# Optimization experiments

Hardware: AMD Instinct MI355X
Metric: run time of the kernel (lower is better)

The kernel has to match this reference:

```python
import jax, jax.numpy as jnp
import numpy as np

PATCH = 3
ALPHA = 0.1


def _unfold3x3(x):
    # x: [B, C, H, W] -> [B, C*9, H, W], torch F.unfold with k=3, pad=1, stride=1
    B, C, H, W = x.shape
    p = PATCH // 2
    xp = jnp.pad(x, ((0, 0), (0, 0), (p, p), (p, p)))
    shifts = [xp[:, :, i:i + H, j:j + W] for i in range(PATCH) for j in range(PATCH)]
    # torch unfold orders (C, kh, kw); ordering is irrelevant for the dot-product
    # correlation, but we match it anyway: stack kernel positions after channel.
    out = jnp.stack(shifts, axis=2)  # [B, C, 9, H, W]
    return out.reshape(B, C * PATCH * PATCH, H, W)


def setup_inputs() -> dict:
    key = jax.random.key(0)
    k1, k2 = jax.random.split(key)
    x_lab = jax.random.normal(k1, (4, 3, 64, 64), dtype=jnp.float32)
    feature = jax.random.normal(k2, (4, 64, 64, 64), dtype=jnp.float32)
    return {"x_lab": x_lab, "feature": feature}


def reference(x_lab, feature):
    # scale_factor=1 and feature already at (H, W): both interpolates are identity.
    B, _, H, W = x_lab.shape
    N = H * W
    x_ab = x_lab.reshape(B, 3, N).transpose(0, 2, 1)          # [B, N, 3]
    lf = _unfold3x3(feature).reshape(B, -1, N)                 # [B, C*9, N]
    corr = jnp.einsum('bcn,bcm->bnm', lf, lf)                  # [B, N, N]
    attn = jax.nn.softmax(corr / ALPHA, axis=-1)
    weighted = jnp.einsum('bnm,bmc->bnc', attn, x_ab)          # [B, N, 3]
    return weighted.transpose(0, 2, 1).reshape(B, 3, H, W)
```

## Files before the change

### kernel.cpp

```cpp
#include <hip/hip_runtime.h>


#define NPIX 4096
#define ROWB  (528 * 16)
#define SCALE 10.0f
#define XCH   1024

typedef __attribute__((ext_vector_type(8))) short bf16x8;
typedef __attribute__((ext_vector_type(4))) float f32x4;

#define MF(a, b, c) __builtin_amdgcn_mfma_f32_16x16x32_bf16(a, b, c, 0, 0, 0)

__device__ __forceinline__ uint4 pack8(const float* v) {
    unsigned h[8];
#pragma unroll
    for (int j = 0; j < 8; ++j) {
        unsigned u = __float_as_uint(v[j]);
        u = u + 0x7fffu + ((u >> 16) & 1u);
        h[j] = u >> 16;
    }
    return (uint4){h[0] | (h[1] << 16), h[2] | (h[3] << 16),
                   h[4] | (h[5] << 16), h[6] | (h[7] << 16)};
}

__device__ __forceinline__ void load_row(const float* fr, int kc, int x, float* L) {
#pragma unroll
    for (int j = 0; j < 8; ++j) L[j] = fr[(size_t)(kc * 8 + j) * NPIX + x];
}

#define MG(T, DBASE, KT) do {                                                 \
    _Pragma("unroll")                                                         \
    for (int dx = 0; dx < 3; ++dx)                                            \
        _Pragma("unroll")                                                     \
        for (int ks = 0; ks < 2; ++ks)                                        \
            acc[T][KT] = MF(AF[((DBASE) + dx) * 2 + ks], B2[ks][dx], acc[T][KT]); \
} while (0)

#define RETIRE(S, myv) do {                                                   \
    _Pragma("unroll")                                                         \
    for (int kt = 0; kt < 4; ++kt) {                                          \
        const int kx = kt * 16 + nl;                                          \
        const float xv0 = xls[(myv) * 64 + kx];                               \
        const float xv1 = xls[XCH + (myv) * 64 + kx];                         \
        const float xv2 = xls[2 * XCH + (myv) * 64 + kx];                     \
        _Pragma("unroll")                                                     \
        for (int rg = 0; rg < 4; ++rg) {                                      \
            const float e = __expf(fmaf(acc[S][kt][rg], SCALE, negM[rg]));    \
            l_[rg] += e;                                                      \
            A0[rg] = fmaf(e, xv0, A0[rg]);                                    \
            A1[rg] = fmaf(e, xv1, A1[rg]);                                    \
            A2[rg] = fmaf(e, xv2, A2[rg]);                                    \
        }                                                                     \
        acc[S][kt] = (f32x4){0.f, 0.f, 0.f, 0.f};                             \
    }                                                                         \
} while (0)

#define STEP(RM, SN, SR, tt) do {                                             \
    const int t_ = (tt);                                                      \
    if (t_ <= 15) {                                                           \
        const int g2 = R0 + 1 + t_;                                           \
        if (g2 < 64) {                                                        \
            float L[8];                                                       \
            load_row(featb + g2 * 64, kc0, x, L);                             \
            *(uint4*)(ring + (SR) * ROWB + wu0) = pack8(L);                   \
            load_row(featb + g2 * 64, kc1, x, L);                             \
            *(uint4*)(ring + (SR) * ROWB + wu1) = pack8(L);                   \
        } else {                                                              \
            *(uint4*)(ring + (SR) * ROWB + wu0) = (uint4){0u, 0u, 0u, 0u};    \
            *(uint4*)(ring + (SR) * ROWB + wu1) = (uint4){0u, 0u, 0u, 0u};    \
        }                                                                     \
    }                                                                         \
    {                                                                         \
        const char* base = ring + (RM) * ROWB + bu;                           \
        _Pragma("unroll")                                                     \
        for (int kt = 0; kt < 4; ++kt) {                                      \
            bf16x8 B2[2][3];                                                  \
            _Pragma("unroll")                                                 \
            for (int ks = 0; ks < 2; ++ks) {                                  \
                const char* p = base + (ks * 264 + kt * 16) * 16;             \
                B2[ks][0] = *(const bf16x8*)(p);                              \
                B2[ks][1] = *(const bf16x8*)(p + 16);                         \
                B2[ks][2] = *(const bf16x8*)(p + 32);                         \
            }                                                                 \
            if (t_ >= 2)              MG(SR, 6, kt);        \
            if (t_ >= 1 && t_ <= 16)  MG(RM, 3, kt);        \
            if (t_ <= 15)             MG(SN, 0, kt);        \
        }                                                                     \
    }                                                                         \
    if (t_ >= 2) RETIRE(SR, t_ - 2);                                          \
    if (t_ < 17) __syncthreads();                                             \
} while (0)

__global__ __launch_bounds__(256)
__attribute__((amdgpu_waves_per_eu(2)))
void nlwa_fused(const float* __restrict__ x_lab,
                const float* __restrict__ feature,
                float4* __restrict__ ws)
{
    __shared__ __align__(16) char ring[3 * ROWB];
    __shared__ float xls[3 * XCH];
    __shared__ float part[3][4][64];
    __shared__ float ssq[3][64];

    const int tid = threadIdx.x;
    const int b = blockIdx.x >> 8;
    const int rem = blockIdx.x & 255;
    const int ny = rem >> 2, kq = rem & 3;
    const int R0 = kq * 16;
    const int w = tid >> 6, lane = tid & 63;
    const int quad = lane >> 4, nl = lane & 15;
    const int kc0 = 2 * w, kc1 = 2 * w + 1;
    const int x = lane;
    const int wu0 = (kc0 * 66 + x + 1) * 16;
    const int wu1 = (kc1 * 66 + x + 1) * 16;
    const int bu = (quad * 66 + nl) * 16;

    const float* featb = feature + (size_t)b * 64 * NPIX;
    const float* xb = x_lab + (size_t)b * 3 * NPIX;

    {
        const int base = R0 * 64;
        float4* d4 = (float4*)xls;
        for (int i = tid; i < 3 * XCH / 4; i += 256) {
            const int ch = i >> 8, off = i & 255;
            d4[i] = *(const float4*)(xb + (size_t)ch * NPIX + base + off * 4);
        }
    }
    if (tid < 48) {
        const int sl = tid / 16, pu = tid % 16;
        const int u = (pu >> 1) * 66 + (pu & 1) * 65;
        *(uint4*)(ring + sl * ROWB + u * 16) = (uint4){0u, 0u, 0u, 0u};
    }

    {
        float L[8];
#pragma unroll
        for (int dyi = 0; dyi < 3; ++dyi) {
            const int qr = ny + dyi - 1;
            float ss = 0.f;
            if (qr >= 0 && qr < 64) {
                load_row(featb + qr * 64, kc0, x, L);
#pragma unroll
                for (int j = 0; j < 8; ++j) ss = fmaf(L[j], L[j], ss);
                *(uint4*)(ring + dyi * ROWB + wu0) = pack8(L);
                load_row(featb + qr * 64, kc1, x, L);
#pragma unroll
                for (int j = 0; j < 8; ++j) ss = fmaf(L[j], L[j], ss);
                *(uint4*)(ring + dyi * ROWB + wu1) = pack8(L);
            } else {
                *(uint4*)(ring + dyi * ROWB + wu0) = (uint4){0u, 0u, 0u, 0u};
                *(uint4*)(ring + dyi * ROWB + wu1) = (uint4){0u, 0u, 0u, 0u};
            }
            part[dyi][w][x] = ss;
        }
    }
    __syncthreads();

    if (tid < 192) {
        const int dyi = tid >> 6, xx = tid & 63;
        float s = 0.f;
#pragma unroll
        for (int k = 0; k < 4; ++k) s += part[dyi][k][xx];
        ssq[dyi][xx] = s;
    }

    bf16x8 AF[18];
#pragma unroll
    for (int dyi = 0; dyi < 3; ++dyi)
#pragma unroll
        for (int dx = 0; dx < 3; ++dx)
#pragma unroll
            for (int ks = 0; ks < 2; ++ks)
                AF[(dyi * 3 + dx) * 2 + ks] = *(const bf16x8*)(ring + dyi * ROWB +
                    ((quad + ks * 4) * 66 + w * 16 + nl + dx) * 16);
    __syncthreads();

    float negM[4];
#pragma unroll
    for (int rg = 0; rg < 4; ++rg) {
        const int q = w * 16 + quad * 4 + rg;
        float a = 0.f;
#pragma unroll
        for (int dyi = 0; dyi < 3; ++dyi)
#pragma unroll
            for (int dx = -1; dx <= 1; ++dx) {
                const int cx = q + dx;
                a += (cx >= 0 && cx < 64) ? ssq[dyi][cx] : 0.f;
            }
        negM[rg] = -SCALE * a;
    }

    {
        float L[8];
#pragma unroll
        for (int rr = 0; rr < 2; ++rr) {
            const int g = R0 - 1 + rr;
            if (g >= 0) {
                load_row(featb + g * 64, kc0, x, L);
                *(uint4*)(ring + rr * ROWB + wu0) = pack8(L);
                load_row(featb + g * 64, kc1, x, L);
                *(uint4*)(ring + rr * ROWB + wu1) = pack8(L);
            } else {
                *(uint4*)(ring + rr * ROWB + wu0) = (uint4){0u, 0u, 0u, 0u};
                *(uint4*)(ring + rr * ROWB + wu1) = (uint4){0u, 0u, 0u, 0u};
            }
        }
    }

    float l_[4], A0[4], A1[4], A2[4];
#pragma unroll
    for (int rg = 0; rg < 4; ++rg) { l_[rg] = 0.f; A0[rg] = 0.f; A1[rg] = 0.f; A2[rg] = 0.f; }
    f32x4 acc[3][4];
#pragma unroll
    for (int i = 0; i < 3; ++i)
#pragma unroll
        for (int kt = 0; kt < 4; ++kt)
            acc[i][kt] = (f32x4){0.f, 0.f, 0.f, 0.f};
    __syncthreads();

    for (int rb = 0; rb < 18; rb += 3) {
        STEP(0, 1, 2, rb);
        STEP(1, 2, 0, rb + 1);
        STEP(2, 0, 1, rb + 2);
    }

#pragma unroll
    for (int rg = 0; rg < 4; ++rg) {
#pragma unroll
        for (int off = 8; off >= 1; off >>= 1) {
            l_[rg] += __shfl_down(l_[rg], off, 16);
            A0[rg] += __shfl_down(A0[rg], off, 16);
            A1[rg] += __shfl_down(A1[rg], off, 16);
            A2[rg] += __shfl_down(A2[rg], off, 16);
        }
    }
    if (nl == 0) {
#pragma unroll
        for (int rg = 0; rg < 4; ++rg) {
            const int q = w * 16 + quad * 4 + rg;
            ws[(size_t)blockIdx.x * 64 + q] =
                make_float4(l_[rg], A0[rg], A1[rg], A2[rg]);
        }
    }
}

__global__ __launch_bounds__(256)
void nlwa_combine(const float4* __restrict__ ws, float* __restrict__ out)
{
    const int i = blockIdx.x * 256 + threadIdx.x;
    const int b = i >> 12, ny = (i >> 6) & 63, q = i & 63;
    const size_t base = ((size_t)(b * 64 + ny) * 4) * 64 + q;
    float4 s = make_float4(0.f, 0.f, 0.f, 0.f);
#pragma unroll
    for (int kq = 0; kq < 4; ++kq) {
        const float4 p = ws[base + (size_t)kq * 64];
        s.x += p.x; s.y += p.y; s.z += p.z; s.w += p.w;
    }
    const float inv = 1.0f / s.x;
    float* o = out + (size_t)b * 3 * NPIX + ny * 64 + q;
    o[0]        = s.y * inv;
    o[NPIX]     = s.z * inv;
    o[2 * NPIX] = s.w * inv;
}

extern "C" void kernel_launch(void* const* d_in, const int* in_sizes, int n_in,
                              void* d_out, int out_size, void* d_ws, size_t ws_size,
                              hipStream_t stream) {
    (void)in_sizes; (void)n_in; (void)out_size; (void)ws_size;
    const float* x_lab   = (const float*)d_in[0];
    const float* feature = (const float*)d_in[1];
    float* out = (float*)d_out;
    float4* ws = (float4*)d_ws;
    nlwa_fused<<<dim3(1024), dim3(256), 0, stream>>>(x_lab, feature, ws);
    nlwa_combine<<<dim3(64), dim3(256), 0, stream>>>(ws, out);
}
```

Baseline: 135.1 us.

## Process two rows per barrier with four-slot LDS ring and early global loads

Restructures the row loop so each super-step handles two feature rows. It issues both rows' global loads up front, runs two MFMA and retire steps, then packs and stores both rows into a four-slot shared ring. This halves the number of __syncthreads and lets global load latency hide behind more compute. In exchange it raises LDS use by one row buffer and keeps more values live in registers, which may hurt occupancy under the two-waves-per-EU constraint.

Result: slower. 413.9 us (+206.5%).

```diff
diff --git a/kernel.cpp b/kernel.cpp
--- a/kernel.cpp
+++ b/kernel.cpp
@@ -55,40 +55,60 @@
     }                                                                         \
 } while (0)
 
-#define STEP(RM, SN, SR, tt) do {                                             \
-    const int t_ = (tt);                                                      \
-    if (t_ <= 15) {                                                           \
-        const int g2 = R0 + 1 + t_;                                           \
-        if (g2 < 64) {                                                        \
-            float L[8];                                                       \
-            load_row(featb + g2 * 64, kc0, x, L);                             \
-            *(uint4*)(ring + (SR) * ROWB + wu0) = pack8(L);                   \
-            load_row(featb + g2 * 64, kc1, x, L);                             \
-            *(uint4*)(ring + (SR) * ROWB + wu1) = pack8(L);                   \
+#define SMFMA(TT) do {                                                        \
+    const char* base_ = ring + ((TT) % 4) * ROWB + bu;                        \
+    _Pragma("unroll")                                                         \
+    for (int kt = 0; kt < 4; ++kt) {                                          \
+        bf16x8 B2[2][3];                                                      \
+        _Pragma("unroll")                                                     \
+        for (int ks = 0; ks < 2; ++ks) {                                      \
+            const char* p = base_ + (ks * 264 + kt * 16) * 16;                \
+            B2[ks][0] = *(const bf16x8*)(p);                                  \
+            B2[ks][1] = *(const bf16x8*)(p + 16);                             \
+            B2[ks][2] = *(const bf16x8*)(p + 32);                             \
+        }                                                                     \
+        if ((TT) >= 2)                MG(((TT) + 2) % 3, 6, kt);              \
+        if ((TT) >= 1 && (TT) <= 16)  MG((TT) % 3,       3, kt);              \
+        if ((TT) <= 15)               MG(((TT) + 1) % 3, 0, kt);              \
+    }                                                                         \
+} while (0)
+
+#define SUPER(TT) do {                                                        \
+    float LA0[8], LA1[8], LB0[8], LB1[8];                                     \
+    const int gA_ = R0 + 1 + (TT), gB_ = R0 + 2 + (TT);                       \
+    if ((TT) <= 15 && gA_ < 64) {                                             \
+        load_row(featb + gA_ * 64, kc0, x, LA0);                              \
+        load_row(featb + gA_ * 64, kc1, x, LA1);                              \
+    }                                                                         \
+    if ((TT) <= 14 && gB_ < 64) {                                             \
+        load_row(featb + gB_ * 64, kc0, x, LB0);                              \
+        load_row(featb + gB_ * 64, kc1, x, LB1);                              \
+    }                                                                         \
+    SMFMA(TT);                                                                \
+    if ((TT) >= 2) RETIRE(((TT) + 2) % 3, (TT) - 2);                          \
+    SMFMA((TT) + 1);                                                          \
+    if ((TT) >= 1) RETIRE((TT) % 3, (TT) - 1);                                \
+    if ((TT) <= 15) {                                                         \
+        char* ws_ = ring + (((TT) + 2) % 4) * ROWB;                           \
+        if (gA_ < 64) {                                                       \
+            *(uint4*)(ws_ + wu0) = pack8(LA0);                                \
+            *(uint4*)(ws_ + wu1) = pack8(LA1);                                \
         } else {                                                              \
-            *(uint4*)(ring + (SR) * ROWB + wu0) = (uint4){0u, 0u, 0u, 0u};    \
-            *(uint4*)(ring + (SR) * ROWB + wu1) = (uint4){0u, 0u, 0u, 0u};    \
-        }                                                                     \
-    }                                                                         \
-    {                                                                         \
-        const char* base = ring + (RM) * ROWB + bu;                           \
-        _Pragma("unroll")                                                     \
-        for (int kt = 0; kt < 4; ++kt) {                                      \
-            bf16x8 B2[2][3];                                                  \
-            _Pragma("unroll")                                                 \
-            for (int ks = 0; ks < 2; ++ks) {                                  \
-                const char* p = base + (ks * 264 + kt * 16) * 16;             \
-                B2[ks][0] = *(const bf16x8*)(p);                              \
-                B2[ks][1] = *(const bf16x8*)(p + 16);                         \
-                B2[ks][2] = *(const bf16x8*)(p + 32);                         \
-            }                                                                 \
-            if (t_ >= 2)              MG(SR, 6, kt);        \
-            if (t_ >= 1 && t_ <= 16)  MG(RM, 3, kt);        \
-            if (t_ <= 15)             MG(SN, 0, kt);        \
-        }                                                                     \
-    }                                                                         \
-    if (t_ >= 2) RETIRE(SR, t_ - 2);                                          \
-    if (t_ < 17) __syncthreads();                                             \
+            *(uint4*)(ws_ + wu0) = (uint4){0u, 0u, 0u, 0u};                   \
+            *(uint4*)(ws_ + wu1) = (uint4){0u, 0u, 0u, 0u};                   \
+        }                                                                     \
+    }                                                                         \
+    if ((TT) <= 14) {                                                         \
+        char* ws_ = ring + (((TT) + 3) % 4) * ROWB;                           \
+        if (gB_ < 64) {                                                       \
+            *(uint4*)(ws_ + wu0) = pack8(LB0);                                \
+            *(uint4*)(ws_ + wu1) = pack8(LB1);                                \
+        } else {                                                              \
+            *(uint4*)(ws_ + wu0) = (uint4){0u, 0u, 0u, 0u};                   \
+            *(uint4*)(ws_ + wu1) = (uint4){0u, 0u, 0u, 0u};                   \
+        }                                                                     \
+    }                                                                         \
+    if ((TT) < 16) __syncthreads();                                           \
 } while (0)
 
 __global__ __launch_bounds__(256)
@@ -97,7 +117,7 @@
                 const float* __restrict__ feature,
                 float4* __restrict__ ws)
 {
-    __shared__ __align__(16) char ring[3 * ROWB];
+    __shared__ __align__(16) char ring[4 * ROWB];
     __shared__ float xls[3 * XCH];
     __shared__ float part[3][4][64];
     __shared__ float ssq[3][64];
@@ -126,7 +146,7 @@
             d4[i] = *(const float4*)(xb + (size_t)ch * NPIX + base + off * 4);
         }
     }
-    if (tid < 48) {
+    if (tid < 64) {
         const int sl = tid / 16, pu = tid % 16;
         const int u = (pu >> 1) * 66 + (pu & 1) * 65;
         *(uint4*)(ring + sl * ROWB + u * 16) = (uint4){0u, 0u, 0u, 0u};
@@ -218,11 +238,8 @@
             acc[i][kt] = (f32x4){0.f, 0.f, 0.f, 0.f};
     __syncthreads();
 
-    for (int rb = 0; rb < 18; rb += 3) {
-        STEP(0, 1, 2, rb);
-        STEP(1, 2, 0, rb + 1);
-        STEP(2, 0, 1, rb + 2);
-    }
+    SUPER(0);  SUPER(2);  SUPER(4);  SUPER(6);  SUPER(8);
+    SUPER(10); SUPER(12); SUPER(14); SUPER(16);
 
 #pragma unroll
     for (int rg = 0; rg < 4; ++rg) {
```

## Pre-convert features to packed bf16 in a separate kernel and defer ring stores

Applied to the files above, without the earlier changes.

Adds a conversion kernel that packs the fp32 feature map into bf16 groups of eight channels in workspace memory once. The fused kernel then loads one 16-byte vector per row instead of eight strided fp32 loads followed by rounding, which cuts global traffic and ALU work per block. The query A fragments now come straight from global memory rather than through the LDS ring, and ring-slot loads are issued before the MFMAs and stored after them to hide load latency. The cost is an extra kernel launch and a full pass over the feature tensor, plus the norm (ssq) is now computed from bf16-rounded values.

Result: faster. 127.9 us (-5.3%).

```diff
diff --git a/kernel.cpp b/kernel.cpp
--- a/kernel.cpp
+++ b/kernel.cpp
@@ -11,22 +11,8 @@
 
 #define MF(a, b, c) __builtin_amdgcn_mfma_f32_16x16x32_bf16(a, b, c, 0, 0, 0)
 
-__device__ __forceinline__ uint4 pack8(const float* v) {
-    unsigned h[8];
-#pragma unroll
-    for (int j = 0; j < 8; ++j) {
-        unsigned u = __float_as_uint(v[j]);
-        u = u + 0x7fffu + ((u >> 16) & 1u);
-        h[j] = u >> 16;
-    }
-    return (uint4){h[0] | (h[1] << 16), h[2] | (h[3] << 16),
-                   h[4] | (h[5] << 16), h[6] | (h[7] << 16)};
-}
-
-__device__ __forceinline__ void load_row(const float* fr, int kc, int x, float* L) {
-#pragma unroll
-    for (int j = 0; j < 8; ++j) L[j] = fr[(size_t)(kc * 8 + j) * NPIX + x];
-}
+__device__ __forceinline__ float blo(unsigned u) { return __uint_as_float(u << 16); }
+__device__ __forceinline__ float bhi(unsigned u) { return __uint_as_float(u & 0xffff0000u); }
 
 #define MG(T, DBASE, KT) do {                                                 \
     _Pragma("unroll")                                                         \
@@ -57,17 +43,12 @@
 
 #define STEP(RM, SN, SR, tt) do {                                             \
     const int t_ = (tt);                                                      \
+    uint4 Rv0 = (uint4){0u, 0u, 0u, 0u}, Rv1 = (uint4){0u, 0u, 0u, 0u};       \
     if (t_ <= 15) {                                                           \
         const int g2 = R0 + 1 + t_;                                           \
         if (g2 < 64) {                                                        \
-            float L[8];                                                       \
-            load_row(featb + g2 * 64, kc0, x, L);                             \
-            *(uint4*)(ring + (SR) * ROWB + wu0) = pack8(L);                   \
-            load_row(featb + g2 * 64, kc1, x, L);                             \
-            *(uint4*)(ring + (SR) * ROWB + wu1) = pack8(L);                   \
-        } else {                                                              \
-            *(uint4*)(ring + (SR) * ROWB + wu0) = (uint4){0u, 0u, 0u, 0u};    \
-            *(uint4*)(ring + (SR) * ROWB + wu1) = (uint4){0u, 0u, 0u, 0u};    \
+            Rv0 = fbb[kc0 * NPIX + g2 * 64 + x];                              \
+            Rv1 = fbb[kc1 * NPIX + g2 * 64 + x];                              \
         }                                                                     \
     }                                                                         \
     {                                                                         \
@@ -82,19 +63,41 @@
                 B2[ks][1] = *(const bf16x8*)(p + 16);                         \
                 B2[ks][2] = *(const bf16x8*)(p + 32);                         \
             }                                                                 \
-            if (t_ >= 2)              MG(SR, 6, kt);        \
-            if (t_ >= 1 && t_ <= 16)  MG(RM, 3, kt);        \
-            if (t_ <= 15)             MG(SN, 0, kt);        \
+            if (t_ >= 2)              MG(((SR)), 6, kt);    \
+            if (t_ >= 1 && t_ <= 16)  MG(((RM)), 3, kt);    \
+            if (t_ <= 15)             MG(((SN)), 0, kt);    \
         }                                                                     \
     }                                                                         \
     if (t_ >= 2) RETIRE(SR, t_ - 2);                                          \
+    if (t_ <= 15) {                                                           \
+        *(uint4*)(ring + (SR) * ROWB + wu0) = Rv0;                            \
+        *(uint4*)(ring + (SR) * ROWB + wu1) = Rv1;                            \
+    }                                                                         \
     if (t_ < 17) __syncthreads();                                             \
 } while (0)
+
+__global__ __launch_bounds__(256)
+void nlwa_convert(const float* __restrict__ feature, uint4* __restrict__ fb)
+{
+    const int idx = blockIdx.x * 256 + threadIdx.x;
+    const int p = idx & (NPIX - 1);
+    const int cb = idx >> 12;
+    const float* src = feature + (size_t)cb * 8 * NPIX + p;
+    unsigned h[8];
+#pragma unroll
+    for (int j = 0; j < 8; ++j) {
+        unsigned u = __float_as_uint(src[(size_t)j * NPIX]);
+        u = u + 0x7fffu + ((u >> 16) & 1u);
+        h[j] = u >> 16;
+    }
+    fb[idx] = (uint4){h[0] | (h[1] << 16), h[2] | (h[3] << 16),
+                      h[4] | (h[5] << 16), h[6] | (h[7] << 16)};
+}
 
 __global__ __launch_bounds__(256)
 __attribute__((amdgpu_waves_per_eu(2)))
 void nlwa_fused(const float* __restrict__ x_lab,
-                const float* __restrict__ feature,
+                const uint4* __restrict__ fb16,
                 float4* __restrict__ ws)
 {
     __shared__ __align__(16) char ring[3 * ROWB];
@@ -115,7 +118,7 @@
     const int wu1 = (kc1 * 66 + x + 1) * 16;
     const int bu = (quad * 66 + nl) * 16;
 
-    const float* featb = feature + (size_t)b * 64 * NPIX;
+    const uint4* fbb = fb16 + (size_t)b * 8 * NPIX;
     const float* xb = x_lab + (size_t)b * 3 * NPIX;
 
     {
@@ -132,27 +135,53 @@
         *(uint4*)(ring + sl * ROWB + u * 16) = (uint4){0u, 0u, 0u, 0u};
     }
 
-    {
-        float L[8];
-#pragma unroll
-        for (int dyi = 0; dyi < 3; ++dyi) {
-            const int qr = ny + dyi - 1;
-            float ss = 0.f;
-            if (qr >= 0 && qr < 64) {
-                load_row(featb + qr * 64, kc0, x, L);
-#pragma unroll
-                for (int j = 0; j < 8; ++j) ss = fmaf(L[j], L[j], ss);
-                *(uint4*)(ring + dyi * ROWB + wu0) = pack8(L);
-                load_row(featb + qr * 64, kc1, x, L);
-#pragma unroll
-                for (int j = 0; j < 8; ++j) ss = fmaf(L[j], L[j], ss);
-                *(uint4*)(ring + dyi * ROWB + wu1) = pack8(L);
-            } else {
-                *(uint4*)(ring + dyi * ROWB + wu0) = (uint4){0u, 0u, 0u, 0u};
-                *(uint4*)(ring + dyi * ROWB + wu1) = (uint4){0u, 0u, 0u, 0u};
+#pragma unroll
+    for (int dyi = 0; dyi < 3; ++dyi) {
+        const int qr = ny + dyi - 1;
+        float ss = 0.f;
+        if (qr >= 0 && qr < 64) {
+            const uint4 v0 = fbb[kc0 * NPIX + qr * 64 + x];
+            const uint4 v1 = fbb[kc1 * NPIX + qr * 64 + x];
+            const unsigned* pv0 = (const unsigned*)&v0;
+            const unsigned* pv1 = (const unsigned*)&v1;
+#pragma unroll
+            for (int d = 0; d < 4; ++d) {
+                float a0 = blo(pv0[d]), a1 = bhi(pv0[d]);
+                float b0 = blo(pv1[d]), b1 = bhi(pv1[d]);
+                ss = fmaf(a0, a0, ss); ss = fmaf(a1, a1, ss);
+                ss = fmaf(b0, b0, ss); ss = fmaf(b1, b1, ss);
             }
-            part[dyi][w][x] = ss;
-        }
+        }
+        part[dyi][w][x] = ss;
+    }
+
+    bf16x8 AF[18];
+#pragma unroll
+    for (int dyi = 0; dyi < 3; ++dyi) {
+        const int qr = ny + dyi - 1;
+#pragma unroll
+        for (int dx = 0; dx < 3; ++dx) {
+            const int cxx = w * 16 + nl + dx - 1;
+#pragma unroll
+            for (int ks = 0; ks < 2; ++ks) {
+                bf16x8 t = (bf16x8){0, 0, 0, 0, 0, 0, 0, 0};
+                if (qr >= 0 && qr < 64 && cxx >= 0 && cxx < 64)
+                    t = *(const bf16x8*)(fbb + (quad + 4 * ks) * NPIX + qr * 64 + cxx);
+                AF[(dyi * 3 + dx) * 2 + ks] = t;
+            }
+        }
+    }
+
+#pragma unroll
+    for (int rr = 0; rr < 2; ++rr) {
+        const int g = R0 - 1 + rr;
+        uint4 v0 = (uint4){0u, 0u, 0u, 0u}, v1 = v0;
+        if (g >= 0) {
+            v0 = fbb[kc0 * NPIX + g * 64 + x];
+            v1 = fbb[kc1 * NPIX + g * 64 + x];
+        }
+        *(uint4*)(ring + rr * ROWB + wu0) = v0;
+        *(uint4*)(ring + rr * ROWB + wu1) = v1;
     }
     __syncthreads();
 
@@ -163,16 +192,6 @@
         for (int k = 0; k < 4; ++k) s += part[dyi][k][xx];
         ssq[dyi][xx] = s;
     }
-
-    bf16x8 AF[18];
-#pragma unroll
-    for (int dyi = 0; dyi < 3; ++dyi)
-#pragma unroll
-        for (int dx = 0; dx < 3; ++dx)
-#pragma unroll
-            for (int ks = 0; ks < 2; ++ks)
-                AF[(dyi * 3 + dx) * 2 + ks] = *(const bf16x8*)(ring + dyi * ROWB +
-                    ((quad + ks * 4) * 66 + w * 16 + nl + dx) * 16);
     __syncthreads();
 
     float negM[4];
@@ -190,23 +209,6 @@
         negM[rg] = -SCALE * a;
     }
 
-    {
-        float L[8];
-#pragma unroll
-        for (int rr = 0; rr < 2; ++rr) {
-            const int g = R0 - 1 + rr;
-            if (g >= 0) {
-                load_row(featb + g * 64, kc0, x, L);
-                *(uint4*)(ring + rr * ROWB + wu0) = pack8(L);
-                load_row(featb + g * 64, kc1, x, L);
-                *(uint4*)(ring + rr * ROWB + wu1) = pack8(L);
-            } else {
-                *(uint4*)(ring + rr * ROWB + wu0) = (uint4){0u, 0u, 0u, 0u};
-                *(uint4*)(ring + rr * ROWB + wu1) = (uint4){0u, 0u, 0u, 0u};
-            }
-        }
-    }
-
     float l_[4], A0[4], A1[4], A2[4];
 #pragma unroll
     for (int rg = 0; rg < 4; ++rg) { l_[rg] = 0.f; A0[rg] = 0.f; A1[rg] = 0.f; A2[rg] = 0.f; }
@@ -216,7 +218,6 @@
 #pragma unroll
         for (int kt = 0; kt < 4; ++kt)
             acc[i][kt] = (f32x4){0.f, 0.f, 0.f, 0.f};
-    __syncthreads();
 
     for (int rb = 0; rb < 18; rb += 3) {
         STEP(0, 1, 2, rb);
@@ -270,7 +271,9 @@
     const float* x_lab   = (const float*)d_in[0];
     const float* feature = (const float*)d_in[1];
     float* out = (float*)d_out;
-    float4* ws = (float4*)d_ws;
-    nlwa_fused<<<dim3(1024), dim3(256), 0, stream>>>(x_lab, feature, ws);
-    nlwa_combine<<<dim3(64), dim3(256), 0, stream>>>(ws, out);
-}
+    float4* wsp = (float4*)d_ws;
+    uint4* fb   = (uint4*)((char*)d_ws + (1 << 20));
+    nlwa_convert<<<dim3(512), dim3(256), 0, stream>>>(feature, fb);
+    nlwa_fused<<<dim3(1024), dim3(256), 0, stream>>>(x_lab, fb, wsp);
+    nlwa_combine<<<dim3(64), dim3(256), 0, stream>>>(wsp, out);
+}
```
